# Kernel tuning notes

Measured on AMD Instinct MI355X. Metric: run time of the kernel, lower is better.

The kernel has to match this reference:

```python
import jax, jax.numpy as jnp
import numpy as np

N_NODES = 100000
N_EDGES = 1200000
IN_FEATS = 64
OUT_FEATS = 32
K_HOPS = 4  # k = len([in_feats] + hidden_lst) with hidden_lst=[64,64,32]


def setup_inputs() -> dict:
    key = jax.random.key(0)
    k1, k2, k3, k4, k5 = jax.random.split(key, 5)
    features = jax.random.normal(k1, (N_NODES, IN_FEATS), dtype=jnp.float32)
    src = jax.random.randint(k2, (N_EDGES,), 0, N_NODES, dtype=jnp.int64)
    dst = jax.random.randint(k3, (N_EDGES,), 0, N_NODES, dtype=jnp.int64)
    # fc layer of SGConv: Linear(in_feats -> out_feats) with bias
    bound = 1.0 / np.sqrt(IN_FEATS)
    W = jax.random.uniform(k4, (OUT_FEATS, IN_FEATS), dtype=jnp.float32,
                           minval=-bound, maxval=bound)
    b = jax.random.uniform(k5, (OUT_FEATS,), dtype=jnp.float32,
                           minval=-bound, maxval=bound)
    return {"features": features, "src": src, "dst": dst, "W": W, "b": b}


def reference(features, src, dst, W, b):
    # DGL SGConv with norm='both': symmetric normalization each hop.
    # in-degree of each dst node, clamped to >= 1
    deg = jax.ops.segment_sum(jnp.ones((N_EDGES,), dtype=features.dtype),
                              dst, num_segments=N_NODES)
    norm = jnp.clip(deg, 1.0, None) ** -0.5  # [N]
    norm = norm[:, None]                      # [N, 1]
    h = features
    for _ in range(K_HOPS):
        h = h * norm                                            # D^{-1/2} x
        h = jax.ops.segment_sum(h[src], dst, num_segments=N_NODES)  # A x (SpMM)
        h = h * norm                                            # D^{-1/2}
    # final linear layer
    return h @ W.T + b
```

## Files before the change

### kernel.cpp

```cpp
#include <hip/hip_runtime.h>
#include <hip/hip_fp16.h>
#include <cstdint>

#define NNODES 100000
#define NEDGES 1200000
#define INF 64
#define OUTF 32
#define SCAN_B 256
#define NBUCK ((NNODES + SCAN_B - 1) / SCAN_B)
#define PCAP 4608
#define BIN_EPT 16
#define BIN_THREADS (NEDGES / BIN_EPT)
#define BIN_BLOCKS ((BIN_THREADS + 255) / 256)
#define PROJ_NPB 16
#define PROJ_BLOCKS (NNODES / PROJ_NPB)
#define CUR_PAD 16

__global__ __launch_bounds__(256) void k_initcur(int* __restrict__ gcur) {
    int i = blockIdx.x * 256 + threadIdx.x;
    if (i < NBUCK) gcur[i * CUR_PAD] = i * PCAP;
}

__global__ __launch_bounds__(256) void k_binproj(const int4* __restrict__ src4,
                                                 const int4* __restrict__ dst4,
                                                 int* __restrict__ gcur,
                                                 unsigned* __restrict__ packed,
                                                 const float4* __restrict__ feat4,
                                                 const float4* __restrict__ W4,
                                                 __half2* __restrict__ h0_p) {
    __shared__ __align__(16) char smem[12480];
    int tid = threadIdx.x;
    if (blockIdx.x < BIN_BLOCKS) {
        int* cnt = (int*)smem;
        int* base = cnt + NBUCK;
        for (int i = tid; i < NBUCK; i += 256) cnt[i] = 0;
        __syncthreads();
        int gid = blockIdx.x * 256 + tid;
        bool act = gid < BIN_THREADS;
        int4 s4[4], d4[4];
        if (act) {
#pragma unroll
            for (int k = 0; k < 4; ++k) {
                s4[k] = src4[(size_t)gid * 4 + k];
                d4[k] = dst4[(size_t)gid * 4 + k];
                atomicAdd(&cnt[d4[k].x >> 8], 1);
                atomicAdd(&cnt[d4[k].y >> 8], 1);
                atomicAdd(&cnt[d4[k].z >> 8], 1);
                atomicAdd(&cnt[d4[k].w >> 8], 1);
            }
        }
        __syncthreads();
        for (int i = tid; i < NBUCK; i += 256) {
            int c = cnt[i];
            base[i] = c ? atomicAdd(&gcur[i * CUR_PAD], c) : 0;
            cnt[i] = 0;
        }
        __syncthreads();
        if (act) {
#pragma unroll
            for (int k = 0; k < 4; ++k) {
                int ss[4] = {s4[k].x, s4[k].y, s4[k].z, s4[k].w};
                int dd[4] = {d4[k].x, d4[k].y, d4[k].z, d4[k].w};
#pragma unroll
                for (int j = 0; j < 4; ++j) {
                    int b = dd[j] >> 8;
                    int rel = atomicAdd(&cnt[b], 1);
                    packed[base[b] + rel] =
                        ((unsigned)(dd[j] & 255) << 17) | (unsigned)ss[j];
                }
            }
        }
    } else {
        float (*Ws)[INF + 1] = (float (*)[INF + 1])smem;
        float (*Fs)[INF + 1] = (float (*)[INF + 1])(smem + 8320);
        int node0 = (blockIdx.x - BIN_BLOCKS) * PROJ_NPB;
        for (int i = tid; i < 512; i += 256) {
            float4 w = W4[i];
            int f = i * 4, of = f >> 6, k = f & 63;
            Ws[of][k] = w.x; Ws[of][k + 1] = w.y;
            Ws[of][k + 2] = w.z; Ws[of][k + 3] = w.w;
        }
        {
            int n = node0 + (tid >> 4), q = tid & 15;
            float4 v = feat4[(size_t)n * 16 + q];
            int c = q * 4;
            Fs[tid >> 4][c] = v.x; Fs[tid >> 4][c + 1] = v.y;
            Fs[tid >> 4][c + 2] = v.z; Fs[tid >> 4][c + 3] = v.w;
        }
        __syncthreads();
        int ln = tid >> 4, n = node0 + ln;
        int of0 = (tid & 15) * 2;
        float a0 = 0.0f, a1 = 0.0f;
#pragma unroll
        for (int k = 0; k < INF; ++k) {
            float f = Fs[ln][k];
            a0 += f * Ws[of0][k];
            a1 += f * Ws[of0 + 1][k];
        }
        h0_p[(size_t)n * 16 + (tid & 15)] = __floats2half2_rn(a0, a1);
    }
}

__global__ __launch_bounds__(256) void k_place(const unsigned* __restrict__ packed,
                                               const int* __restrict__ gcur,
                                               int* __restrict__ col,
                                               int2* __restrict__ rowse,
                                               float* __restrict__ norm) {
    __shared__ unsigned sin_[PCAP];
    __shared__ int stage[PCAP];
    __shared__ int deg[SCAN_B];
    __shared__ int rs[SCAN_B];
    int b = blockIdx.x, tid = threadIdx.x;
    int node0 = b * SCAN_B;
    int nn = (NNODES - node0 < SCAN_B) ? (NNODES - node0) : SCAN_B;
    int ebase = b * PCAP;
    int nedge = gcur[b * CUR_PAD] - ebase;
    deg[tid] = 0;
    __syncthreads();
    for (int i = tid; i < nedge; i += 256) {
        unsigned pk = packed[ebase + i];
        sin_[i] = pk;
        atomicAdd(&deg[pk >> 17], 1);
    }
    __syncthreads();
    int d = deg[tid];
    rs[tid] = d;
    __syncthreads();
    for (int st = 1; st < SCAN_B; st <<= 1) {
        int add = (tid >= st) ? rs[tid - st] : 0;
        __syncthreads();
        rs[tid] += add;
        __syncthreads();
    }
    int myoff = rs[tid] - d;
    if (tid < nn) {
        norm[node0 + tid] = rsqrtf(d < 1 ? 1.0f : (float)d);
        rowse[node0 + tid] = make_int2(ebase + myoff, ebase + myoff + d);
    }
    deg[tid] = myoff;
    __syncthreads();
    for (int i = tid; i < nedge; i += 256) {
        unsigned pk = sin_[i];
        int rel = atomicAdd(&deg[pk >> 17], 1);
        stage[rel] = (int)(pk & 0x1FFFFu);
    }
    __syncthreads();
    for (int i = tid; i < nedge; i += 256) col[ebase + i] = stage[i];
}

template <bool FIRST, bool LAST>
__global__ __launch_bounds__(256) void k_gather(const uint2* __restrict__ uin,
                                                void* __restrict__ uout,
                                                const int2* __restrict__ rowse,
                                                const int* __restrict__ col,
                                                const float* __restrict__ norm,
                                                const float4* __restrict__ bias4) {
    int t = blockIdx.x * 256 + threadIdx.x;
    int node = t >> 3;
    if (node >= NNODES) return;
    int lane = t & 7;
    int2 se = rowse[node];
    int e = se.x, re = se.y;
    float4 acc = make_float4(0.f, 0.f, 0.f, 0.f);
    auto accum = [&](uint2 r, float w) {
        float2 f01 = __half22float2(*(const __half2*)&r.x);
        float2 f23 = __half22float2(*(const __half2*)&r.y);
        acc.x += w * f01.x; acc.y += w * f01.y;
        acc.z += w * f23.x; acc.w += w * f23.y;
    };
    for (; e + 7 < re; e += 8) {
        int s0 = col[e],     s1 = col[e + 1], s2 = col[e + 2], s3 = col[e + 3];
        int s4 = col[e + 4], s5 = col[e + 5], s6 = col[e + 6], s7 = col[e + 7];
        uint2 r0 = uin[(size_t)s0 * 8 + lane];
        uint2 r1 = uin[(size_t)s1 * 8 + lane];
        uint2 r2 = uin[(size_t)s2 * 8 + lane];
        uint2 r3 = uin[(size_t)s3 * 8 + lane];
        uint2 r4 = uin[(size_t)s4 * 8 + lane];
        uint2 r5 = uin[(size_t)s5 * 8 + lane];
        uint2 r6 = uin[(size_t)s6 * 8 + lane];
        uint2 r7 = uin[(size_t)s7 * 8 + lane];
        if (FIRST) {
            accum(r0, norm[s0]); accum(r1, norm[s1]);
            accum(r2, norm[s2]); accum(r3, norm[s3]);
            accum(r4, norm[s4]); accum(r5, norm[s5]);
            accum(r6, norm[s6]); accum(r7, norm[s7]);
        } else {
            accum(r0, 1.f); accum(r1, 1.f); accum(r2, 1.f); accum(r3, 1.f);
            accum(r4, 1.f); accum(r5, 1.f); accum(r6, 1.f); accum(r7, 1.f);
        }
    }
    for (; e < re; ++e) {
        int s = col[e];
        accum(uin[(size_t)s * 8 + lane], FIRST ? norm[s] : 1.f);
    }
    float nn = norm[node];
    float w = LAST ? nn : nn * nn;
    acc.x *= w; acc.y *= w; acc.z *= w; acc.w *= w;
    if (LAST) {
        float4 bb = bias4[lane];
        acc.x += bb.x; acc.y += bb.y; acc.z += bb.z; acc.w += bb.w;
        ((float4*)uout)[(size_t)node * 8 + lane] = acc;
    } else {
        uint2 r;
        *(__half2*)&r.x = __floats2half2_rn(acc.x, acc.y);
        *(__half2*)&r.y = __floats2half2_rn(acc.z, acc.w);
        ((uint2*)uout)[(size_t)node * 8 + lane] = r;
    }
}

extern "C" void kernel_launch(void* const* d_in, const int* in_sizes, int n_in,
                              void* d_out, int out_size, void* d_ws, size_t ws_size,
                              hipStream_t stream) {
    const float* feat = (const float*)d_in[0];
    const int*   src  = (const int*)d_in[1];
    const int*   dst  = (const int*)d_in[2];
    const float* W    = (const float*)d_in[3];
    const float* b    = (const float*)d_in[4];
    float* out = (float*)d_out;

    char* ws = (char*)d_ws;
    size_t off = 0;
    auto alloc = [&](size_t bytes) {
        void* p = ws + off;
        off = (off + bytes + 255) & ~(size_t)255;
        return p;
    };
    float*    norm   = (float*)alloc((size_t)NNODES * 4);
    int2*     rowse  = (int2*)alloc((size_t)NNODES * 8);
    int*      gcur   = (int*)alloc((size_t)NBUCK * CUR_PAD * 4);
    unsigned* packed = (unsigned*)alloc((size_t)NBUCK * PCAP * 4);
    int*      col    = (int*)alloc((size_t)NBUCK * PCAP * 4);
    void*     h0     = alloc((size_t)NNODES * OUTF * 2);
    void*     h1     = alloc((size_t)NNODES * OUTF * 2);

    k_initcur<<<(NBUCK + 255) / 256, 256, 0, stream>>>(gcur);
    k_binproj<<<BIN_BLOCKS + PROJ_BLOCKS, 256, 0, stream>>>(
        (const int4*)src, (const int4*)dst, gcur, packed,
        (const float4*)feat, (const float4*)W, (__half2*)h0);
    k_place<<<NBUCK, 256, 0, stream>>>(packed, gcur, col, rowse, norm);

    const int ggrid = (NNODES * 8 + 255) / 256;
    k_gather<true,  false><<<ggrid, 256, 0, stream>>>(
        (const uint2*)h0, h1, rowse, col, norm, nullptr);
    k_gather<false, false><<<ggrid, 256, 0, stream>>>(
        (const uint2*)h1, h0, rowse, col, norm, nullptr);
    k_gather<false, false><<<ggrid, 256, 0, stream>>>(
        (const uint2*)h0, h1, rowse, col, norm, nullptr);
    k_gather<false, true><<<ggrid, 256, 0, stream>>>(
        (const uint2*)h1, out, rowse, col, norm, (const float4*)b);
}
```

Measured before the change: 138.8 us.

## Widen gather to 4 lanes per node with uint4 loads and prescale h0

The gather kernels now use 4 threads per node, each loading 16 bytes (8 halves) per neighbor instead of 8 threads loading 8 bytes. The first hop's per-source norm multiply is moved into a separate prescale kernel over h0, so every gather is a plain sum. Row start and degree are packed into one 32-bit word, which halves the row metadata read per node. The projection inner loop is also vectorised to float2 shared-memory reads. This adds an extra kernel launch and a pass over h0, and the packing limits degree to 2047 and edge offsets to 21 bits.

```diff
diff --git a/kernel.cpp b/kernel.cpp
--- a/kernel.cpp
+++ b/kernel.cpp
@@ -15,6 +15,7 @@
 #define PROJ_NPB 16
 #define PROJ_BLOCKS (NNODES / PROJ_NPB)
 #define CUR_PAD 16
+#define WST 66
 
 __global__ __launch_bounds__(256) void k_initcur(int* __restrict__ gcur) {
     int i = blockIdx.x * 256 + threadIdx.x;
@@ -28,7 +29,7 @@
                                                  const float4* __restrict__ feat4,
                                                  const float4* __restrict__ W4,
                                                  __half2* __restrict__ h0_p) {
-    __shared__ __align__(16) char smem[12480];
+    __shared__ __align__(16) char smem[12672];
     int tid = threadIdx.x;
     if (blockIdx.x < BIN_BLOCKS) {
         int* cnt = (int*)smem;
@@ -71,8 +72,8 @@
             }
         }
     } else {
-        float (*Ws)[INF + 1] = (float (*)[INF + 1])smem;
-        float (*Fs)[INF + 1] = (float (*)[INF + 1])(smem + 8320);
+        float (*Ws)[WST] = (float (*)[WST])smem;
+        float (*Fs)[WST] = (float (*)[WST])(smem + 32 * WST * 4);
         int node0 = (blockIdx.x - BIN_BLOCKS) * PROJ_NPB;
         for (int i = tid; i < 512; i += 256) {
             float4 w = W4[i];
@@ -90,12 +91,15 @@
         __syncthreads();
         int ln = tid >> 4, n = node0 + ln;
         int of0 = (tid & 15) * 2;
+        const float2* fp = (const float2*)&Fs[ln][0];
+        const float2* w0 = (const float2*)&Ws[of0][0];
+        const float2* w1 = (const float2*)&Ws[of0 + 1][0];
         float a0 = 0.0f, a1 = 0.0f;
 #pragma unroll
-        for (int k = 0; k < INF; ++k) {
-            float f = Fs[ln][k];
-            a0 += f * Ws[of0][k];
-            a1 += f * Ws[of0 + 1][k];
+        for (int k2 = 0; k2 < 32; ++k2) {
+            float2 f = fp[k2], x = w0[k2], y = w1[k2];
+            a0 += f.x * x.x + f.y * x.y;
+            a1 += f.x * y.x + f.y * y.y;
         }
         h0_p[(size_t)n * 16 + (tid & 15)] = __floats2half2_rn(a0, a1);
     }
@@ -104,7 +108,7 @@
 __global__ __launch_bounds__(256) void k_place(const unsigned* __restrict__ packed,
                                                const int* __restrict__ gcur,
                                                int* __restrict__ col,
-                                               int2* __restrict__ rowse,
+                                               unsigned* __restrict__ rowsd,
                                                float* __restrict__ norm) {
     __shared__ unsigned sin_[PCAP];
     __shared__ int stage[PCAP];
@@ -135,7 +139,7 @@
     int myoff = rs[tid] - d;
     if (tid < nn) {
         norm[node0 + tid] = rsqrtf(d < 1 ? 1.0f : (float)d);
-        rowse[node0 + tid] = make_int2(ebase + myoff, ebase + myoff + d);
+        rowsd[node0 + tid] = ((unsigned)(ebase + myoff) << 11) | (unsigned)d;
     }
     deg[tid] = myoff;
     __syncthreads();
@@ -148,63 +152,81 @@
     for (int i = tid; i < nedge; i += 256) col[ebase + i] = stage[i];
 }
 
-template <bool FIRST, bool LAST>
-__global__ __launch_bounds__(256) void k_gather(const uint2* __restrict__ uin,
+__global__ __launch_bounds__(256) void k_scale(uint4* __restrict__ h0,
+                                               const float* __restrict__ norm) {
+    int i = blockIdx.x * 256 + threadIdx.x;
+    if (i >= NNODES * 4) return;
+    float nn = norm[i >> 2];
+    uint4 r = h0[i];
+    float2 f0 = __half22float2(*(const __half2*)&r.x);
+    float2 f1 = __half22float2(*(const __half2*)&r.y);
+    float2 f2 = __half22float2(*(const __half2*)&r.z);
+    float2 f3 = __half22float2(*(const __half2*)&r.w);
+    *(__half2*)&r.x = __floats2half2_rn(nn * f0.x, nn * f0.y);
+    *(__half2*)&r.y = __floats2half2_rn(nn * f1.x, nn * f1.y);
+    *(__half2*)&r.z = __floats2half2_rn(nn * f2.x, nn * f2.y);
+    *(__half2*)&r.w = __floats2half2_rn(nn * f3.x, nn * f3.y);
+    h0[i] = r;
+}
+
+template <bool LAST>
+__global__ __launch_bounds__(256) void k_gather(const uint4* __restrict__ uin,
                                                 void* __restrict__ uout,
-                                                const int2* __restrict__ rowse,
+                                                const unsigned* __restrict__ rowsd,
                                                 const int* __restrict__ col,
                                                 const float* __restrict__ norm,
                                                 const float4* __restrict__ bias4) {
     int t = blockIdx.x * 256 + threadIdx.x;
-    int node = t >> 3;
+    int node = t >> 2;
     if (node >= NNODES) return;
-    int lane = t & 7;
-    int2 se = rowse[node];
-    int e = se.x, re = se.y;
-    float4 acc = make_float4(0.f, 0.f, 0.f, 0.f);
-    auto accum = [&](uint2 r, float w) {
-        float2 f01 = __half22float2(*(const __half2*)&r.x);
-        float2 f23 = __half22float2(*(const __half2*)&r.y);
-        acc.x += w * f01.x; acc.y += w * f01.y;
-        acc.z += w * f23.x; acc.w += w * f23.y;
+    int lane = t & 3;
+    unsigned rd = rowsd[node];
+    int e = rd >> 11;
+    int re = e + (int)(rd & 2047u);
+    const uint4* up = uin + lane;
+    float4 accA = make_float4(0.f, 0.f, 0.f, 0.f);
+    float4 accB = make_float4(0.f, 0.f, 0.f, 0.f);
+    auto add = [&](uint4 r) {
+        float2 f0 = __half22float2(*(const __half2*)&r.x);
+        float2 f1 = __half22float2(*(const __half2*)&r.y);
+        float2 f2 = __half22float2(*(const __half2*)&r.z);
+        float2 f3 = __half22float2(*(const __half2*)&r.w);
+        accA.x += f0.x; accA.y += f0.y; accA.z += f1.x; accA.w += f1.y;
+        accB.x += f2.x; accB.y += f2.y; accB.z += f3.x; accB.w += f3.y;
     };
     for (; e + 7 < re; e += 8) {
         int s0 = col[e],     s1 = col[e + 1], s2 = col[e + 2], s3 = col[e + 3];
         int s4 = col[e + 4], s5 = col[e + 5], s6 = col[e + 6], s7 = col[e + 7];
-        uint2 r0 = uin[(size_t)s0 * 8 + lane];
-        uint2 r1 = uin[(size_t)s1 * 8 + lane];
-        uint2 r2 = uin[(size_t)s2 * 8 + lane];
-        uint2 r3 = uin[(size_t)s3 * 8 + lane];
-        uint2 r4 = uin[(size_t)s4 * 8 + lane];
-        uint2 r5 = uin[(size_t)s5 * 8 + lane];
-        uint2 r6 = uin[(size_t)s6 * 8 + lane];
-        uint2 r7 = uin[(size_t)s7 * 8 + lane];
-        if (FIRST) {
-            accum(r0, norm[s0]); accum(r1, norm[s1]);
-            accum(r2, norm[s2]); accum(r3, norm[s3]);
-            accum(r4, norm[s4]); accum(r5, norm[s5]);
-            accum(r6, norm[s6]); accum(r7, norm[s7]);
-        } else {
-            accum(r0, 1.f); accum(r1, 1.f); accum(r2, 1.f); accum(r3, 1.f);
-            accum(r4, 1.f); accum(r5, 1.f); accum(r6, 1.f); accum(r7, 1.f);
-        }
-    }
-    for (; e < re; ++e) {
-        int s = col[e];
-        accum(uin[(size_t)s * 8 + lane], FIRST ? norm[s] : 1.f);
-    }
+        uint4 r0 = up[(size_t)s0 * 4];
+        uint4 r1 = up[(size_t)s1 * 4];
+        uint4 r2 = up[(size_t)s2 * 4];
+        uint4 r3 = up[(size_t)s3 * 4];
+        uint4 r4 = up[(size_t)s4 * 4];
+        uint4 r5 = up[(size_t)s5 * 4];
+        uint4 r6 = up[(size_t)s6 * 4];
+        uint4 r7 = up[(size_t)s7 * 4];
+        add(r0); add(r1); add(r2); add(r3);
+        add(r4); add(r5); add(r6); add(r7);
+    }
+    for (; e < re; ++e) add(up[(size_t)col[e] * 4]);
     float nn = norm[node];
     float w = LAST ? nn : nn * nn;
-    acc.x *= w; acc.y *= w; acc.z *= w; acc.w *= w;
+    accA.x *= w; accA.y *= w; accA.z *= w; accA.w *= w;
+    accB.x *= w; accB.y *= w; accB.z *= w; accB.w *= w;
     if (LAST) {
-        float4 bb = bias4[lane];
-        acc.x += bb.x; acc.y += bb.y; acc.z += bb.z; acc.w += bb.w;
-        ((float4*)uout)[(size_t)node * 8 + lane] = acc;
+        float4 b0 = bias4[lane * 2], b1 = bias4[lane * 2 + 1];
+        accA.x += b0.x; accA.y += b0.y; accA.z += b0.z; accA.w += b0.w;
+        accB.x += b1.x; accB.y += b1.y; accB.z += b1.z; accB.w += b1.w;
+        float4* o = (float4*)uout;
+        o[(size_t)node * 8 + lane * 2]     = accA;
+        o[(size_t)node * 8 + lane * 2 + 1] = accB;
     } else {
-        uint2 r;
-        *(__half2*)&r.x = __floats2half2_rn(acc.x, acc.y);
-        *(__half2*)&r.y = __floats2half2_rn(acc.z, acc.w);
-        ((uint2*)uout)[(size_t)node * 8 + lane] = r;
+        uint4 r;
+        *(__half2*)&r.x = __floats2half2_rn(accA.x, accA.y);
+        *(__half2*)&r.y = __floats2half2_rn(accA.z, accA.w);
+        *(__half2*)&r.z = __floats2half2_rn(accB.x, accB.y);
+        *(__half2*)&r.w = __floats2half2_rn(accB.z, accB.w);
+        ((uint4*)uout)[(size_t)node * 4 + lane] = r;
     }
 }
 
@@ -226,7 +248,7 @@
         return p;
     };
     float*    norm   = (float*)alloc((size_t)NNODES * 4);
-    int2*     rowse  = (int2*)alloc((size_t)NNODES * 8);
+    unsigned* rowsd  = (unsigned*)alloc((size_t)NNODES * 4);
     int*      gcur   = (int*)alloc((size_t)NBUCK * CUR_PAD * 4);
     unsigned* packed = (unsigned*)alloc((size_t)NBUCK * PCAP * 4);
     int*      col    = (int*)alloc((size_t)NBUCK * PCAP * 4);
@@ -237,15 +259,17 @@
     k_binproj<<<BIN_BLOCKS + PROJ_BLOCKS, 256, 0, stream>>>(
         (const int4*)src, (const int4*)dst, gcur, packed,
         (const float4*)feat, (const float4*)W, (__half2*)h0);
-    k_place<<<NBUCK, 256, 0, stream>>>(packed, gcur, col, rowse, norm);
-
-    const int ggrid = (NNODES * 8 + 255) / 256;
-    k_gather<true,  false><<<ggrid, 256, 0, stream>>>(
-        (const uint2*)h0, h1, rowse, col, norm, nullptr);
-    k_gather<false, false><<<ggrid, 256, 0, stream>>>(
-        (const uint2*)h1, h0, rowse, col, norm, nullptr);
-    k_gather<false, false><<<ggrid, 256, 0, stream>>>(
-        (const uint2*)h0, h1, rowse, col, norm, nullptr);
-    k_gather<false, true><<<ggrid, 256, 0, stream>>>(
-        (const uint2*)h1, out, rowse, col, norm, (const float4*)b);
-}
+    k_place<<<NBUCK, 256, 0, stream>>>(packed, gcur, col, rowsd, norm);
+
+    const int sgrid = (NNODES * 4 + 255) / 256;
+    k_scale<<<sgrid, 256, 0, stream>>>((uint4*)h0, norm);
+
+    k_gather<false><<<sgrid, 256, 0, stream>>>(
+        (const uint4*)h0, h1, rowsd, col, norm, nullptr);
+    k_gather<false><<<sgrid, 256, 0, stream>>>(
+        (const uint4*)h1, h0, rowsd, col, norm, nullptr);
+    k_gather<false><<<sgrid, 256, 0, stream>>>(
+        (const uint4*)h0, h1, rowsd, col, norm, nullptr);
+    k_gather<true><<<sgrid, 256, 0, stream>>>(
+        (const uint4*)h1, out, rowsd, col, norm, (const float4*)b);
+}
```

Measured after the change: 140.6 us. About the same (+1.3%).
